# Optimization experiments

Hardware: AMD Instinct MI355X
Metric: run time of the kernel (lower is better)

Reference implementation:

```python
import jax, jax.numpy as jnp
import numpy as np

WIN = 11
K1 = 0.01
K2 = 0.03


def setup_inputs() -> dict:
    key = jax.random.key(0)
    k1, k2 = jax.random.split(key)
    B, C, H, W = 64, 1, 512, 512
    img = jax.random.uniform(k1, (B, C, H, W), dtype=jnp.float32)
    ref = jax.random.uniform(k2, (B, C, H, W), dtype=jnp.float32)
    data_range = jnp.ones((B,), dtype=jnp.float32)
    return {"img": img, "ref": ref, "data_range": data_range}


def _box_filter(x, win):
    w = jnp.ones((1, 1, win, win), dtype=x.dtype) / (win * win)
    pad = win // 2
    return jax.lax.conv_general_dilated(
        x, w, window_strides=(1, 1),
        padding=[(pad, pad), (pad, pad)],
        dimension_numbers=("NCHW", "OIHW", "NCHW"))


def reference(img, ref, data_range):
    dr = data_range[:, None, None, None]
    C1 = (K1 * dr) ** 2
    C2 = (K2 * dr) ** 2
    n_pix = WIN * WIN
    cov_norm = n_pix / (n_pix - 1)

    ux = _box_filter(img, WIN)
    uy = _box_filter(ref, WIN)
    uxx = _box_filter(img * img, WIN)
    uyy = _box_filter(ref * ref, WIN)
    uxy = _box_filter(img * ref, WIN)

    vx = cov_norm * (uxx - ux * ux)
    vy = cov_norm * (uyy - uy * uy)
    vxy = cov_norm * (uxy - ux * uy)

    A1 = 2 * ux * uy + C1
    A2 = 2 * vxy + C2
    B1 = ux ** 2 + uy ** 2 + C1
    B2 = vx + vy + C2
    S = A1 * A2 / (B1 * B2)
    return S
```

## Files before the change

kernel.cpp:

```cpp
#include <hip/hip_runtime.h>


static constexpr int WIN_  = 11;
static constexpr int RS    = 32;
static constexpr int HI    = 512;
static constexpr int WI    = 512;
static constexpr int HALO  = 8;
static constexpr int LDSW  = 544;

__global__ __launch_bounds__(256, 2)
void ssim_fused(const float* __restrict__ img, const float* __restrict__ ref,
                const float* __restrict__ drng, float* __restrict__ out)
{
  const int t  = threadIdx.x;
  const int r0 = (int)blockIdx.x * RS;
  const int b  = (int)blockIdx.y;

  __shared__ __align__(16) float sV[5][LDSW];
  for (int k = t; k < 5 * LDSW; k += 256) (&sV[0][0])[k] = 0.0f;

  const float dr  = drng[b];
  const float C1  = (0.01f * dr) * (0.01f * dr);
  const float C2  = (0.03f * dr) * (0.03f * dr);
  const float inv_n    = 1.0f / 121.0f;
  const float cov_norm = 121.0f / 120.0f;

  const size_t base = (size_t)b * ((size_t)HI * WI);
  const float* imgb = img + base;
  const float* refb = ref + base;

  float xh[WIN_][2], yh[WIN_][2];
#pragma unroll
  for (int k = 0; k < WIN_; ++k) { xh[k][0]=0.f; xh[k][1]=0.f; yh[k][0]=0.f; yh[k][1]=0.f; }
  float Sx[2]={0.f,0.f}, Sy[2]={0.f,0.f}, Sxx[2]={0.f,0.f}, Syy[2]={0.f,0.f}, Sxy[2]={0.f,0.f};

  __syncthreads();

  for (int ib = 0; ib < 4; ++ib) {
#pragma unroll
    for (int j = 0; j < WIN_; ++j) {
      const int i = ib * WIN_ + j;
      if (i < RS + 10) {
        const int ri = r0 - 5 + i;
        float xv0=0.f, xv1=0.f, yv0=0.f, yv1=0.f;
        if (ri >= 0 && ri < HI) {
          const float2 xv = *(const float2*)(imgb + (size_t)ri * WI + 2*t);
          const float2 yv = *(const float2*)(refb + (size_t)ri * WI + 2*t);
          xv0=xv.x; xv1=xv.y; yv0=yv.x; yv1=yv.y;
        }
        Sx[0]+=xv0; Sx[1]+=xv1; Sy[0]+=yv0; Sy[1]+=yv1;
        Sxx[0]=fmaf(xv0,xv0,Sxx[0]); Sxx[1]=fmaf(xv1,xv1,Sxx[1]);
        Syy[0]=fmaf(yv0,yv0,Syy[0]); Syy[1]=fmaf(yv1,yv1,Syy[1]);
        Sxy[0]=fmaf(xv0,yv0,Sxy[0]); Sxy[1]=fmaf(xv1,yv1,Sxy[1]);

        const int ci = HALO + 2*t;
        *(float2*)&sV[0][ci] = make_float2(Sx[0],  Sx[1]);
        *(float2*)&sV[1][ci] = make_float2(Sy[0],  Sy[1]);
        *(float2*)&sV[2][ci] = make_float2(Sxx[0], Sxx[1]);
        *(float2*)&sV[3][ci] = make_float2(Syy[0], Syy[1]);
        *(float2*)&sV[4][ci] = make_float2(Sxy[0], Sxy[1]);

        {
          const int jo = (j + 1) % WIN_;
          const float xo0=xh[jo][0], xo1=xh[jo][1], yo0=yh[jo][0], yo1=yh[jo][1];
          Sx[0]-=xo0; Sx[1]-=xo1; Sy[0]-=yo0; Sy[1]-=yo1;
          Sxx[0]=fmaf(-xo0,xo0,Sxx[0]); Sxx[1]=fmaf(-xo1,xo1,Sxx[1]);
          Syy[0]=fmaf(-yo0,yo0,Syy[0]); Syy[1]=fmaf(-yo1,yo1,Syy[1]);
          Sxy[0]=fmaf(-xo0,yo0,Sxy[0]); Sxy[1]=fmaf(-xo1,yo1,Sxy[1]);
          xh[j][0]=xv0; xh[j][1]=xv1; yh[j][0]=yv0; yh[j][1]=yv1;
        }

        __syncthreads();

        if (i >= 10 && t < 128) {
          const int ro = ri - 5;
          const int c0 = 4 * t;
          float H[5][4];
#pragma unroll
          for (int q = 0; q < 5; ++q) {
            const float4* p = (const float4*)&sV[q][c0];
            const float4 va = p[0], vb = p[1], vc = p[2], vd = p[3], ve = p[4];
            const float v3=va.w,  v4=vb.x,  v5=vb.y,  v6=vb.z,  v7=vb.w,
                        v8=vc.x,  v9=vc.y,  v10=vc.z, v11=vc.w,
                        v12=vd.x, v13=vd.y, v14=vd.z, v15=vd.w, v16=ve.x;
            const float w0 = ((v3+v4)+(v5+v6)) + ((v7+v8)+(v9+v10)) + ((v11+v12)+v13);
            const float w1 = w0 - v3 + v14;
            const float w2 = w1 - v4 + v15;
            const float w3 = w2 - v5 + v16;
            H[q][0]=w0; H[q][1]=w1; H[q][2]=w2; H[q][3]=w3;
          }
          float4 res;
          float* rp = (float*)&res;
#pragma unroll
          for (int k = 0; k < 4; ++k) {
            const float ux = H[0][k]*inv_n, uy  = H[1][k]*inv_n;
            const float uxx= H[2][k]*inv_n, uyy = H[3][k]*inv_n, uxy = H[4][k]*inv_n;
            const float vx = cov_norm*(uxx - ux*ux);
            const float vy = cov_norm*(uyy - uy*uy);
            const float vxy= cov_norm*(uxy - ux*uy);
            const float A1 = 2.f*ux*uy + C1;
            const float A2 = 2.f*vxy + C2;
            const float B1 = ux*ux + uy*uy + C1;
            const float B2 = vx + vy + C2;
            rp[k] = (A1*A2) * __builtin_amdgcn_rcpf(B1*B2);
          }
          *(float4*)(out + ((size_t)b*HI + ro)*WI + c0) = res;
        }
        __syncthreads();
      }
    }
  }
}

extern "C" void kernel_launch(void* const* d_in, const int* in_sizes, int n_in,
                              void* d_out, int out_size, void* d_ws, size_t ws_size,
                              hipStream_t stream)
{
  const float* img = (const float*)d_in[0];
  const float* ref = (const float*)d_in[1];
  const float* drg = (const float*)d_in[2];
  float* out = (float*)d_out;
  const int B = in_sizes[0] / (HI * WI);
  dim3 grid(HI / RS, B);
  dim3 block(256);
  hipLaunchKernelGGL(ssim_fused, grid, block, 0, stream, img, ref, drg, out);
}
```

Before: 247.3 us.

## Replace LDS block SSIM with per-wavefront strips using shuffle horizontal sums

The kernel is restructured so that each 64-lane wavefront independently handles an 8-row strip of one full image row. Each lane owns 8 columns. The horizontal 11-tap box sum now uses cross-lane shuffles instead of shared memory, which removes the LDS buffer and all block-wide barriers. The vertical sliding window no longer keeps an 11-row register history; it re-reads the row leaving the window from global memory. The short strips add a 10-row halo per 8 output rows, roughly doubling the input reads (much of it likely hitting cache), in exchange for more parallelism and no synchronization.

```diff
diff --git a/kernel.cpp b/kernel.cpp
--- a/kernel.cpp
+++ b/kernel.cpp
@@ -1,23 +1,40 @@
 #include <hip/hip_runtime.h>
 
 
-static constexpr int WIN_  = 11;
-static constexpr int RS    = 32;
-static constexpr int HI    = 512;
-static constexpr int WI    = 512;
-static constexpr int HALO  = 8;
-static constexpr int LDSW  = 544;
+static constexpr int HI = 512, WI = 512;
+static constexpr int RS = 8;
+static constexpr int STRIPS = HI / RS;
 
-__global__ __launch_bounds__(256, 2)
-void ssim_fused(const float* __restrict__ img, const float* __restrict__ ref,
-                const float* __restrict__ drng, float* __restrict__ out)
+__device__ __forceinline__ void horiz11(const float v[8], float H[8], int lane) {
+  float L[5], R[5];
+#pragma unroll
+  for (int k = 0; k < 5; ++k) {
+    float lt = __shfl(v[3 + k], (lane + 63) & 63);
+    L[k] = (lane == 0) ? 0.f : lt;
+    float rt = __shfl(v[k], (lane + 1) & 63);
+    R[k] = (lane == 63) ? 0.f : rt;
+  }
+  float h = (((L[0] + L[1]) + (L[2] + L[3])) + ((L[4] + v[0]) + (v[1] + v[2])))
+            + ((v[3] + v[4]) + v[5]);
+  H[0] = h;
+  h = h - L[0] + v[6]; H[1] = h;
+  h = h - L[1] + v[7]; H[2] = h;
+  h = h - L[2] + R[0]; H[3] = h;
+  h = h - L[3] + R[1]; H[4] = h;
+  h = h - L[4] + R[2]; H[5] = h;
+  h = h - v[0] + R[3]; H[6] = h;
+  h = h - v[1] + R[4]; H[7] = h;
+}
+
+__global__ __launch_bounds__(256, 3)
+void ssim_wave(const float* __restrict__ img, const float* __restrict__ ref,
+               const float* __restrict__ drng, float* __restrict__ out)
 {
-  const int t  = threadIdx.x;
-  const int r0 = (int)blockIdx.x * RS;
-  const int b  = (int)blockIdx.y;
-
-  __shared__ __align__(16) float sV[5][LDSW];
-  for (int k = t; k < 5 * LDSW; k += 256) (&sV[0][0])[k] = 0.0f;
+  const int lane = threadIdx.x & 63;
+  const int wv   = (int)blockIdx.x * 4 + (threadIdx.x >> 6);
+  const int b    = wv >> 6;
+  const int r0   = (wv & (STRIPS - 1)) * RS;
+  const int c0   = lane * 8;
 
   const float dr  = drng[b];
   const float C1  = (0.01f * dr) * (0.01f * dr);
@@ -26,88 +43,82 @@
   const float cov_norm = 121.0f / 120.0f;
 
   const size_t base = (size_t)b * ((size_t)HI * WI);
-  const float* imgb = img + base;
-  const float* refb = ref + base;
+  const float* xb = img + base;
+  const float* yb = ref + base;
+  float*       ob = out + base;
 
-  float xh[WIN_][2], yh[WIN_][2];
+  float Sx[8], Sy[8], Sxx[8], Syy[8], Sxy[8];
 #pragma unroll
-  for (int k = 0; k < WIN_; ++k) { xh[k][0]=0.f; xh[k][1]=0.f; yh[k][0]=0.f; yh[k][1]=0.f; }
-  float Sx[2]={0.f,0.f}, Sy[2]={0.f,0.f}, Sxx[2]={0.f,0.f}, Syy[2]={0.f,0.f}, Sxy[2]={0.f,0.f};
+  for (int c = 0; c < 8; ++c) { Sx[c]=0.f; Sy[c]=0.f; Sxx[c]=0.f; Syy[c]=0.f; Sxy[c]=0.f; }
 
-  __syncthreads();
+  for (int i = 0; i < RS + 10; ++i) {
+    const int ri = r0 - 5 + i;
+    float xn[8], yn[8], xo[8], yo[8];
 
-  for (int ib = 0; ib < 4; ++ib) {
+    if (ri >= 0 && ri < HI) {
+      const float4* px = (const float4*)(xb + (size_t)ri * WI + c0);
+      const float4* py = (const float4*)(yb + (size_t)ri * WI + c0);
+      const float4 a0 = px[0], a1 = px[1];
+      const float4 b0 = py[0], b1 = py[1];
+      xn[0]=a0.x; xn[1]=a0.y; xn[2]=a0.z; xn[3]=a0.w;
+      xn[4]=a1.x; xn[5]=a1.y; xn[6]=a1.z; xn[7]=a1.w;
+      yn[0]=b0.x; yn[1]=b0.y; yn[2]=b0.z; yn[3]=b0.w;
+      yn[4]=b1.x; yn[5]=b1.y; yn[6]=b1.z; yn[7]=b1.w;
+    } else {
 #pragma unroll
-    for (int j = 0; j < WIN_; ++j) {
-      const int i = ib * WIN_ + j;
-      if (i < RS + 10) {
-        const int ri = r0 - 5 + i;
-        float xv0=0.f, xv1=0.f, yv0=0.f, yv1=0.f;
-        if (ri >= 0 && ri < HI) {
-          const float2 xv = *(const float2*)(imgb + (size_t)ri * WI + 2*t);
-          const float2 yv = *(const float2*)(refb + (size_t)ri * WI + 2*t);
-          xv0=xv.x; xv1=xv.y; yv0=yv.x; yv1=yv.y;
-        }
-        Sx[0]+=xv0; Sx[1]+=xv1; Sy[0]+=yv0; Sy[1]+=yv1;
-        Sxx[0]=fmaf(xv0,xv0,Sxx[0]); Sxx[1]=fmaf(xv1,xv1,Sxx[1]);
-        Syy[0]=fmaf(yv0,yv0,Syy[0]); Syy[1]=fmaf(yv1,yv1,Syy[1]);
-        Sxy[0]=fmaf(xv0,yv0,Sxy[0]); Sxy[1]=fmaf(xv1,yv1,Sxy[1]);
+      for (int c = 0; c < 8; ++c) { xn[c]=0.f; yn[c]=0.f; }
+    }
 
-        const int ci = HALO + 2*t;
-        *(float2*)&sV[0][ci] = make_float2(Sx[0],  Sx[1]);
-        *(float2*)&sV[1][ci] = make_float2(Sy[0],  Sy[1]);
-        *(float2*)&sV[2][ci] = make_float2(Sxx[0], Sxx[1]);
-        *(float2*)&sV[3][ci] = make_float2(Syy[0], Syy[1]);
-        *(float2*)&sV[4][ci] = make_float2(Sxy[0], Sxy[1]);
+    const int rold = ri - 11;
+    if (i >= 11 && rold >= 0) {
+      const float4* px = (const float4*)(xb + (size_t)rold * WI + c0);
+      const float4* py = (const float4*)(yb + (size_t)rold * WI + c0);
+      const float4 a0 = px[0], a1 = px[1];
+      const float4 b0 = py[0], b1 = py[1];
+      xo[0]=a0.x; xo[1]=a0.y; xo[2]=a0.z; xo[3]=a0.w;
+      xo[4]=a1.x; xo[5]=a1.y; xo[6]=a1.z; xo[7]=a1.w;
+      yo[0]=b0.x; yo[1]=b0.y; yo[2]=b0.z; yo[3]=b0.w;
+      yo[4]=b1.x; yo[5]=b1.y; yo[6]=b1.z; yo[7]=b1.w;
+    } else {
+#pragma unroll
+      for (int c = 0; c < 8; ++c) { xo[c]=0.f; yo[c]=0.f; }
+    }
 
-        {
-          const int jo = (j + 1) % WIN_;
-          const float xo0=xh[jo][0], xo1=xh[jo][1], yo0=yh[jo][0], yo1=yh[jo][1];
-          Sx[0]-=xo0; Sx[1]-=xo1; Sy[0]-=yo0; Sy[1]-=yo1;
-          Sxx[0]=fmaf(-xo0,xo0,Sxx[0]); Sxx[1]=fmaf(-xo1,xo1,Sxx[1]);
-          Syy[0]=fmaf(-yo0,yo0,Syy[0]); Syy[1]=fmaf(-yo1,yo1,Syy[1]);
-          Sxy[0]=fmaf(-xo0,yo0,Sxy[0]); Sxy[1]=fmaf(-xo1,yo1,Sxy[1]);
-          xh[j][0]=xv0; xh[j][1]=xv1; yh[j][0]=yv0; yh[j][1]=yv1;
-        }
+#pragma unroll
+    for (int c = 0; c < 8; ++c) {
+      Sx[c]  += xn[c] - xo[c];
+      Sy[c]  += yn[c] - yo[c];
+      Sxx[c] = fmaf(xn[c], xn[c], fmaf(-xo[c], xo[c], Sxx[c]));
+      Syy[c] = fmaf(yn[c], yn[c], fmaf(-yo[c], yo[c], Syy[c]));
+      Sxy[c] = fmaf(xn[c], yn[c], fmaf(-xo[c], yo[c], Sxy[c]));
+    }
 
-        __syncthreads();
+    if (i >= 10) {
+      float H0[8], H1[8], H2[8], H3[8], H4[8];
+      horiz11(Sx,  H0, lane);
+      horiz11(Sy,  H1, lane);
+      horiz11(Sxx, H2, lane);
+      horiz11(Syy, H3, lane);
+      horiz11(Sxy, H4, lane);
 
-        if (i >= 10 && t < 128) {
-          const int ro = ri - 5;
-          const int c0 = 4 * t;
-          float H[5][4];
+      float res[8];
 #pragma unroll
-          for (int q = 0; q < 5; ++q) {
-            const float4* p = (const float4*)&sV[q][c0];
-            const float4 va = p[0], vb = p[1], vc = p[2], vd = p[3], ve = p[4];
-            const float v3=va.w,  v4=vb.x,  v5=vb.y,  v6=vb.z,  v7=vb.w,
-                        v8=vc.x,  v9=vc.y,  v10=vc.z, v11=vc.w,
-                        v12=vd.x, v13=vd.y, v14=vd.z, v15=vd.w, v16=ve.x;
-            const float w0 = ((v3+v4)+(v5+v6)) + ((v7+v8)+(v9+v10)) + ((v11+v12)+v13);
-            const float w1 = w0 - v3 + v14;
-            const float w2 = w1 - v4 + v15;
-            const float w3 = w2 - v5 + v16;
-            H[q][0]=w0; H[q][1]=w1; H[q][2]=w2; H[q][3]=w3;
-          }
-          float4 res;
-          float* rp = (float*)&res;
-#pragma unroll
-          for (int k = 0; k < 4; ++k) {
-            const float ux = H[0][k]*inv_n, uy  = H[1][k]*inv_n;
-            const float uxx= H[2][k]*inv_n, uyy = H[3][k]*inv_n, uxy = H[4][k]*inv_n;
-            const float vx = cov_norm*(uxx - ux*ux);
-            const float vy = cov_norm*(uyy - uy*uy);
-            const float vxy= cov_norm*(uxy - ux*uy);
-            const float A1 = 2.f*ux*uy + C1;
-            const float A2 = 2.f*vxy + C2;
-            const float B1 = ux*ux + uy*uy + C1;
-            const float B2 = vx + vy + C2;
-            rp[k] = (A1*A2) * __builtin_amdgcn_rcpf(B1*B2);
-          }
-          *(float4*)(out + ((size_t)b*HI + ro)*WI + c0) = res;
-        }
-        __syncthreads();
+      for (int c = 0; c < 8; ++c) {
+        const float ux  = H0[c] * inv_n, uy  = H1[c] * inv_n;
+        const float uxx = H2[c] * inv_n, uyy = H3[c] * inv_n, uxy = H4[c] * inv_n;
+        const float vx  = cov_norm * (uxx - ux * ux);
+        const float vy  = cov_norm * (uyy - uy * uy);
+        const float vxy = cov_norm * (uxy - ux * uy);
+        const float A1 = 2.f * ux * uy + C1;
+        const float A2 = 2.f * vxy + C2;
+        const float B1 = ux * ux + uy * uy + C1;
+        const float B2 = vx + vy + C2;
+        res[c] = (A1 * A2) * __builtin_amdgcn_rcpf(B1 * B2);
       }
+      const int ro = ri - 5;
+      float4* po = (float4*)(ob + (size_t)ro * WI + c0);
+      po[0] = make_float4(res[0], res[1], res[2], res[3]);
+      po[1] = make_float4(res[4], res[5], res[6], res[7]);
     }
   }
 }
@@ -121,7 +132,8 @@
   const float* drg = (const float*)d_in[2];
   float* out = (float*)d_out;
   const int B = in_sizes[0] / (HI * WI);
-  dim3 grid(HI / RS, B);
+  const int waves = B * STRIPS;
+  dim3 grid(waves / 4);
   dim3 block(256);
-  hipLaunchKernelGGL(ssim_fused, grid, block, 0, stream, img, ref, drg, out);
+  hipLaunchKernelGGL(ssim_wave, grid, block, 0, stream, img, ref, drg, out);
 }
```

New measurement: 210.9 us. -14.7%, faster.
